# Optimization experiments

Hardware: AMD Instinct MI355X
Metric: run time of the kernel (lower is better)

Reference implementation:

```python
import jax, jax.numpy as jnp
import numpy as np

N, C = 65536, 100
TEMP = 2.0


def setup_inputs() -> dict:
    key = jax.random.key(0)
    ks = jax.random.split(key, 7)
    inp = {}
    names = ["outputs1", "outputs2", "outputs3", "outputs4", "outputs5", "mimic"]
    for k, name in zip(ks[:6], names):
        inp[name] = jax.random.normal(k, (N, C), dtype=jnp.float32)
    inp["targets"] = jax.random.randint(ks[6], (N,), 0, C, dtype=jnp.int64)
    inp["n_test"] = N
    return inp


def _margin(x, targets):
    # top-2 values per row; margin = top1-top2 if the target class is the argmax, else 0
    top2, _ = jax.lax.top_k(x, 2)  # [N, 2]
    tgt_val = jnp.take_along_axis(x, targets[:, None], axis=1)[:, 0]  # [N]
    return jnp.where(tgt_val == top2[:, 0], top2[:, 0] - top2[:, 1],
                     jnp.zeros((), dtype=x.dtype))


def reference(outputs1, outputs2, outputs3, outputs4, outputs5, mimic, targets, n_test):
    margins = jnp.stack(
        [_margin(o, targets) for o in (outputs1, outputs2, outputs3, outputs4, outputs5, mimic)],
        axis=-1,
    )  # [n_test, 6]
    out_threshold = jax.nn.softmax(margins / TEMP, axis=-1)
    max_preds = jnp.max(jnp.stack([outputs1, outputs2, outputs3, outputs4, outputs5], axis=0))
    return (max_preds, out_threshold)
```

## Files before the change

### kernel.cpp

```cpp
#include <hip/hip_runtime.h>


constexpr int C = 100;
constexpr float INV_TEMP = 0.5f;

__device__ __forceinline__ unsigned enc_f(float f) {
    unsigned u = __float_as_uint(f);
    return (u & 0x80000000u) ? ~u : (u | 0x80000000u);
}

__global__ void setup_kernel(unsigned* __restrict__ ws) {
    ws[0] = 0x007FFFFFu;
}

__global__ __launch_bounds__(256) void margin_softmax_kernel(
    const float* __restrict__ o1, const float* __restrict__ o2,
    const float* __restrict__ o3, const float* __restrict__ o4,
    const float* __restrict__ o5, const float* __restrict__ mimic,
    const int* __restrict__ tgt, float* __restrict__ out,
    unsigned* __restrict__ ws, int n)
{
    const float* mats[6] = {o1, o2, o3, o4, o5, mimic};
    const int tid  = blockIdx.x * blockDim.x + threadIdx.x;
    const int lane = threadIdx.x & 63;

    const int idx   = 2 * lane + 1;
    const int probe = (idx < n) ? tgt[idx] : 0;
    const unsigned long long nz = __ballot(probe != 0);
    const int tstride = (nz == 0ull) ? 2 : 1;

    float gmax = -INFINITY;

    if (tid < n) {
        const size_t rowoff = (size_t)tid * C;
        const int t = tgt[(size_t)tid * tstride];

        float margins[6];
        #pragma unroll
        for (int m = 0; m < 6; ++m) {
            const float4* __restrict__ p4 = (const float4*)(mats[m] + rowoff);
            float m1a = -INFINITY, m2a = -INFINITY;
            float m1b = -INFINITY, m2b = -INFINITY;
            #pragma unroll
            for (int i = 0; i < C / 4; ++i) {
                float4 v = p4[i];
                m2a = fmaxf(m2a, fminf(m1a, v.x)); m1a = fmaxf(m1a, v.x);
                m2b = fmaxf(m2b, fminf(m1b, v.y)); m1b = fmaxf(m1b, v.y);
                m2a = fmaxf(m2a, fminf(m1a, v.z)); m1a = fmaxf(m1a, v.z);
                m2b = fmaxf(m2b, fminf(m1b, v.w)); m1b = fmaxf(m1b, v.w);
            }
            const float m1 = fmaxf(m1a, m1b);
            const float m2 = fmaxf(fminf(m1a, m1b), fmaxf(m2a, m2b));
            const float tv = mats[m][rowoff + t];
            margins[m] = (tv == m1) ? (m1 - m2) * INV_TEMP : 0.0f;
            if (m < 5) gmax = fmaxf(gmax, m1);
        }

        float mx = margins[0];
        #pragma unroll
        for (int j = 1; j < 6; ++j) mx = fmaxf(mx, margins[j]);
        float e[6], s = 0.0f;
        #pragma unroll
        for (int j = 0; j < 6; ++j) { e[j] = __expf(margins[j] - mx); s += e[j]; }
        const float inv = 1.0f / s;
        #pragma unroll
        for (int j = 0; j < 6; ++j) out[1 + (size_t)tid * 6 + j] = e[j] * inv;
    }

    #pragma unroll
    for (int s = 1; s < 64; s <<= 1) gmax = fmaxf(gmax, __shfl_xor(gmax, s));
    if (lane == 0) atomicMax(ws, enc_f(gmax));
}

__global__ void finalize_kernel(const unsigned* __restrict__ ws, float* __restrict__ out) {
    unsigned e = ws[0];
    unsigned bits = (e & 0x80000000u) ? (e & 0x7FFFFFFFu) : ~e;
    out[0] = __uint_as_float(bits);
}

extern "C" void kernel_launch(void* const* d_in, const int* in_sizes, int n_in,
                              void* d_out, int out_size, void* d_ws, size_t ws_size,
                              hipStream_t stream) {
    const float* o1    = (const float*)d_in[0];
    const float* o2    = (const float*)d_in[1];
    const float* o3    = (const float*)d_in[2];
    const float* o4    = (const float*)d_in[3];
    const float* o5    = (const float*)d_in[4];
    const float* mimic = (const float*)d_in[5];
    const int*   tgt   = (const int*)d_in[6];
    float*       out   = (float*)d_out;
    unsigned*    ws    = (unsigned*)d_ws;

    const int n = in_sizes[6];

    setup_kernel<<<1, 1, 0, stream>>>(ws);
    const int blocks = (n + 255) / 256;
    margin_softmax_kernel<<<blocks, 256, 0, stream>>>(o1, o2, o3, o4, o5, mimic,
                                                      tgt, out, ws, n);
    finalize_kernel<<<1, 1, 0, stream>>>(ws, out);
}
```

Measured before the change: 204.5 us.

## Split margin computation across matrices via 2D grid, then separate softmax pass

The fused per-row kernel is split in two. A margin kernel uses a 2D grid with blockIdx.y selecting one of the six matrices, so each thread scans one row of one matrix. A second kernel then applies the softmax over the six margins and writes the global max, which replaces the finalize kernel. The aim is six times more parallelism and fewer serial loads per thread. The cost is an extra round trip of the margins through global memory, more atomics, and strided 6-float stores from the margin kernel.

New measurement: 218.1 us. 1.07x slower.

```diff
diff --git a/kernel.cpp b/kernel.cpp
--- a/kernel.cpp
+++ b/kernel.cpp
@@ -13,16 +13,20 @@
     ws[0] = 0x007FFFFFu;
 }
 
-__global__ __launch_bounds__(256) void margin_softmax_kernel(
+__global__ __launch_bounds__(256) void margin_kernel(
     const float* __restrict__ o1, const float* __restrict__ o2,
     const float* __restrict__ o3, const float* __restrict__ o4,
     const float* __restrict__ o5, const float* __restrict__ mimic,
     const int* __restrict__ tgt, float* __restrict__ out,
     unsigned* __restrict__ ws, int n)
 {
-    const float* mats[6] = {o1, o2, o3, o4, o5, mimic};
-    const int tid  = blockIdx.x * blockDim.x + threadIdx.x;
+    const int m    = blockIdx.y;
+    const int row  = blockIdx.x * blockDim.x + threadIdx.x;
     const int lane = threadIdx.x & 63;
+
+    const float* __restrict__ mat =
+        (m == 0) ? o1 : (m == 1) ? o2 : (m == 2) ? o3 :
+        (m == 3) ? o4 : (m == 4) ? o5 : mimic;
 
     const int idx   = 2 * lane + 1;
     const int probe = (idx < n) ? tgt[idx] : 0;
@@ -31,51 +35,58 @@
 
     float gmax = -INFINITY;
 
-    if (tid < n) {
-        const size_t rowoff = (size_t)tid * C;
-        const int t = tgt[(size_t)tid * tstride];
+    if (row < n) {
+        const size_t rowoff = (size_t)row * C;
+        const float4* __restrict__ p4 = (const float4*)(mat + rowoff);
+        float m1a = -INFINITY, m2a = -INFINITY;
+        float m1b = -INFINITY, m2b = -INFINITY;
+        #pragma unroll
+        for (int i = 0; i < C / 4; ++i) {
+            float4 v = p4[i];
+            m2a = fmaxf(m2a, fminf(m1a, v.x)); m1a = fmaxf(m1a, v.x);
+            m2b = fmaxf(m2b, fminf(m1b, v.y)); m1b = fmaxf(m1b, v.y);
+            m2a = fmaxf(m2a, fminf(m1a, v.z)); m1a = fmaxf(m1a, v.z);
+            m2b = fmaxf(m2b, fminf(m1b, v.w)); m1b = fmaxf(m1b, v.w);
+        }
+        const float m1 = fmaxf(m1a, m1b);
+        const float m2 = fmaxf(fminf(m1a, m1b), fmaxf(m2a, m2b));
+        const int   t  = tgt[(size_t)row * tstride];
+        const float tv = mat[rowoff + t];
+        out[1 + (size_t)row * 6 + m] = (tv == m1) ? (m1 - m2) * INV_TEMP : 0.0f;
+        if (m < 5) gmax = m1;
+    }
 
-        float margins[6];
+    if (m < 5) {
         #pragma unroll
-        for (int m = 0; m < 6; ++m) {
-            const float4* __restrict__ p4 = (const float4*)(mats[m] + rowoff);
-            float m1a = -INFINITY, m2a = -INFINITY;
-            float m1b = -INFINITY, m2b = -INFINITY;
-            #pragma unroll
-            for (int i = 0; i < C / 4; ++i) {
-                float4 v = p4[i];
-                m2a = fmaxf(m2a, fminf(m1a, v.x)); m1a = fmaxf(m1a, v.x);
-                m2b = fmaxf(m2b, fminf(m1b, v.y)); m1b = fmaxf(m1b, v.y);
-                m2a = fmaxf(m2a, fminf(m1a, v.z)); m1a = fmaxf(m1a, v.z);
-                m2b = fmaxf(m2b, fminf(m1b, v.w)); m1b = fmaxf(m1b, v.w);
-            }
-            const float m1 = fmaxf(m1a, m1b);
-            const float m2 = fmaxf(fminf(m1a, m1b), fmaxf(m2a, m2b));
-            const float tv = mats[m][rowoff + t];
-            margins[m] = (tv == m1) ? (m1 - m2) * INV_TEMP : 0.0f;
-            if (m < 5) gmax = fmaxf(gmax, m1);
-        }
+        for (int s = 1; s < 64; s <<= 1) gmax = fmaxf(gmax, __shfl_xor(gmax, s));
+        if (lane == 0) atomicMax(ws, enc_f(gmax));
+    }
+}
 
-        float mx = margins[0];
+__global__ __launch_bounds__(256) void softmax_kernel(
+    float* __restrict__ out, const unsigned* __restrict__ ws, int n)
+{
+    const int row = blockIdx.x * blockDim.x + threadIdx.x;
+    if (row < n) {
+        float* p = out + 1 + (size_t)row * 6;
+        float mrg[6];
         #pragma unroll
-        for (int j = 1; j < 6; ++j) mx = fmaxf(mx, margins[j]);
+        for (int j = 0; j < 6; ++j) mrg[j] = p[j];
+        float mx = mrg[0];
+        #pragma unroll
+        for (int j = 1; j < 6; ++j) mx = fmaxf(mx, mrg[j]);
         float e[6], s = 0.0f;
         #pragma unroll
-        for (int j = 0; j < 6; ++j) { e[j] = __expf(margins[j] - mx); s += e[j]; }
+        for (int j = 0; j < 6; ++j) { e[j] = __expf(mrg[j] - mx); s += e[j]; }
         const float inv = 1.0f / s;
         #pragma unroll
-        for (int j = 0; j < 6; ++j) out[1 + (size_t)tid * 6 + j] = e[j] * inv;
+        for (int j = 0; j < 6; ++j) p[j] = e[j] * inv;
     }
-
-    #pragma unroll
-    for (int s = 1; s < 64; s <<= 1) gmax = fmaxf(gmax, __shfl_xor(gmax, s));
-    if (lane == 0) atomicMax(ws, enc_f(gmax));
-}
-
-__global__ void finalize_kernel(const unsigned* __restrict__ ws, float* __restrict__ out) {
-    unsigned e = ws[0];
-    unsigned bits = (e & 0x80000000u) ? (e & 0x7FFFFFFFu) : ~e;
-    out[0] = __uint_as_float(bits);
+    if (row == 0) {
+        unsigned e = ws[0];
+        unsigned bits = (e & 0x80000000u) ? (e & 0x7FFFFFFFu) : ~e;
+        out[0] = __uint_as_float(bits);
+    }
 }
 
 extern "C" void kernel_launch(void* const* d_in, const int* in_sizes, int n_in,
@@ -94,8 +105,8 @@
     const int n = in_sizes[6];
 
     setup_kernel<<<1, 1, 0, stream>>>(ws);
-    const int blocks = (n + 255) / 256;
-    margin_softmax_kernel<<<blocks, 256, 0, stream>>>(o1, o2, o3, o4, o5, mimic,
-                                                      tgt, out, ws, n);
-    finalize_kernel<<<1, 1, 0, stream>>>(ws, out);
+    dim3 grid((n + 255) / 256, 6);
+    margin_kernel<<<grid, 256, 0, stream>>>(o1, o2, o3, o4, o5, mimic,
+                                            tgt, out, ws, n);
+    softmax_kernel<<<(n + 255) / 256, 256, 0, stream>>>(out, ws, n);
 }
```
